# Kernel optimization log

Measured on AMD Instinct MI355X. Metric: run time of the kernel, lower is better.

Reference implementation:

```python
import jax, jax.numpy as jnp
import numpy as np

N = 50000
C_IN = 64
C_OUT = 64
K = 16
EPS = 1e-5


def _bn(x, g, b, m, v):
    # eval-mode BatchNorm1d over last dim
    return (x - m) * jax.lax.rsqrt(v + EPS) * g + b


def setup_inputs() -> dict:
    key = jax.random.key(0)
    ks = jax.random.split(key, 24)
    def lin(i, fan_in, fan_out):
        s = 1.0 / np.sqrt(fan_in)
        W = jax.random.uniform(ks[i], (fan_in, fan_out), jnp.float32, -s, s)
        b = jax.random.uniform(ks[i + 1], (fan_out,), jnp.float32, -s, s)
        return W, b
    Wq, bq = lin(0, C_IN, C_OUT)
    Wk, bk = lin(2, C_IN, C_OUT)
    Wv, bv = lin(4, C_IN, C_OUT)
    Wp, b_p = lin(6, 3, C_OUT)
    Wg1, bg1 = lin(8, C_OUT, C_OUT)
    Wg2, bg2 = lin(10, C_OUT, C_OUT)
    Wo, bo = lin(12, C_OUT, C_OUT)
    def bn_params(i):
        g = jax.random.uniform(ks[i], (C_OUT,), jnp.float32, 0.5, 1.5)
        b = jax.random.normal(ks[i + 1], (C_OUT,), jnp.float32) * 0.1
        m = jax.random.normal(ks[i + 2], (C_OUT,), jnp.float32) * 0.1
        v = jax.random.uniform(ks[i + 3], (C_OUT,), jnp.float32, 0.5, 1.5)
        return g, b, m, v
    bnp_g, bnp_b, bnp_m, bnp_v = bn_params(14)
    bng_g, bng_b, bng_m, bng_v = bn_params(18)
    points = jax.random.normal(ks[22], (N, 3), jnp.float32)
    features = jax.random.normal(ks[23], (N, C_IN), jnp.float32)
    grouped_indices = jax.random.randint(jax.random.fold_in(key, 7), (N, K), 0, N, jnp.int64 if jax.config.jax_enable_x64 else jnp.int32)
    return dict(points=points, features=features, grouped_indices=grouped_indices,
                Wq=Wq, bq=bq, Wk=Wk, bk=bk, Wv=Wv, bv=bv, Wp=Wp, b_p=b_p,
                bnp_g=bnp_g, bnp_b=bnp_b, bnp_m=bnp_m, bnp_v=bnp_v,
                Wg1=Wg1, bg1=bg1, bng_g=bng_g, bng_b=bng_b, bng_m=bng_m, bng_v=bng_v,
                Wg2=Wg2, bg2=bg2, Wo=Wo, bo=bo)


def reference(points, features, grouped_indices,
              Wq, bq, Wk, bk, Wv, bv, Wp, b_p,
              bnp_g, bnp_b, bnp_m, bnp_v,
              Wg1, bg1, bng_g, bng_b, bng_m, bng_v,
              Wg2, bg2, Wo, bo):
    q = features @ Wq + bq                      # (N, C)
    k = features @ Wk + bk
    v = features @ Wv + bv
    gpts = points[grouped_indices]              # (N, K, 3) gather
    gk = k[grouped_indices]                     # (N, K, C)
    gv = v[grouped_indices]                     # (N, K, C)
    rel = gpts - points[:, None, :]             # (N, K, 3)
    p = jax.nn.relu(_bn(rel @ Wp + b_p, bnp_g, bnp_b, bnp_m, bnp_v))  # (N, K, C)
    a = q[:, None, :] - gk + p                  # (N, K, C)
    h = jax.nn.relu(_bn(a @ Wg1 + bg1, bng_g, bng_b, bng_m, bng_v)) @ Wg2 + bg2
    attn = jax.nn.softmax(h, axis=1)            # softmax over neighbor axis
    out = jnp.sum((gv + p) * attn, axis=1) @ Wo + bo  # (N, C)
    return out
```

## Files before the change

kernel.cpp:

```cpp
#include <hip/hip_runtime.h>
#include <hip/hip_bf16.h>

#define EPSV 1e-5f
#define TW 4
#define TPW 8
#define SPD 76

typedef __attribute__((ext_vector_type(8))) short s8v;
typedef __attribute__((ext_vector_type(4))) float f4v;

struct InP {
  const float *points, *features; const int* gidx;
  const float *Wq,*bq,*Wk,*bk,*Wv,*bv,*Wp,*b_p;
  const float *bnp_g,*bnp_b,*bnp_m,*bnp_v;
  const float *Wg1,*bg1,*bng_g,*bng_b,*bng_m,*bng_v;
  const float *Wg2,*bg2,*Wo,*bo;
  float* out; int N;
};
struct WS {
  unsigned short *qW1;
  unsigned short *kvT;
  unsigned short *WAf, *Wkf, *Wvf, *W1f, *W2f, *Wof;
  unsigned short *Wpf;
  float *bq1F, *bpF, *bk1F;
};

__device__ __forceinline__ unsigned short f2bf(float x){
  __hip_bfloat16 h = __float2bfloat16(x);
  unsigned short u; __builtin_memcpy(&u, &h, 2); return u;
}
__device__ __forceinline__ float bf2f(unsigned short s){
  union{unsigned u; float f;} c; c.u = ((unsigned)s) << 16; return c.f;
}
__device__ __forceinline__ unsigned pk2(float x, float y){
  __hip_bfloat162 h = __float22bfloat162_rn(make_float2(x, y));
  unsigned u; __builtin_memcpy(&u, &h, 4); return u;
}
__device__ __forceinline__ s8v pack8(f4v x0, f4v x1){
  s8v r;
  ((unsigned*)&r)[0] = pk2(x0[0], x0[1]);
  ((unsigned*)&r)[1] = pk2(x0[2], x0[3]);
  ((unsigned*)&r)[2] = pk2(x1[0], x1[1]);
  ((unsigned*)&r)[3] = pk2(x1[2], x1[3]);
  return r;
}

__global__ void __launch_bounds__(256) prep_kernel(InP P, WS W){
  const int g = blockIdx.x*256 + threadIdx.x;
  const int e = g >> 3, j = g & 7;
  const int f = e >> 6, L = e & 63;
  const int ks = f & 1, nt = f >> 1;
  const int n = nt*16 + (L & 15);
  const int k = ks*32 + ((L >> 4) << 3) + j;
  const float sg = P.bng_g[n] * rsqrtf(P.bng_v[n] + EPSV);
  W.W1f[e*8+j] = f2bf(P.Wg1[k*64+n] * sg);
  W.W2f[e*8+j] = f2bf(P.Wg2[k*64+n]);
  W.Wof[e*8+j] = f2bf(P.Wo [k*64+n]);
  W.Wvf[e*8+j] = f2bf(P.Wv [k*64+n]);
  float acc = 0.f, acck = 0.f;
  #pragma unroll 8
  for (int d = 0; d < 64; d++){
    float w1 = P.Wg1[d*64+n];
    acc  += P.Wq[k*64+d] * w1;
    acck += P.Wk[k*64+d] * w1;
  }
  W.WAf[e*8+j] = f2bf(acc  * sg);
  W.Wkf[e*8+j] = f2bf(acck * sg);
  if (g < 2048){
    int ep = g >> 3;
    int ntp = ep >> 6, Lp = ep & 63;
    int np_ = ntp*16 + (Lp & 15);
    int kp = ((Lp >> 4) << 3) + j;
    float sp = P.bnp_g[np_] * rsqrtf(P.bnp_v[np_] + EPSV);
    W.Wpf[ep*8+j] = f2bf(kp < 3 ? P.Wp[kp*64+np_]*sp : 0.f);
  }
  if (g < 64){
    float sgt = P.bng_g[g] * rsqrtf(P.bng_v[g] + EPSV);
    float spt = P.bnp_g[g] * rsqrtf(P.bnp_v[g] + EPSV);
    float acc2 = 0.f, acck2 = 0.f;
    for (int d = 0; d < 64; d++){
      float w1 = P.Wg1[d*64+g];
      acc2  += P.bq[d] * w1;
      acck2 += P.bk[d] * w1;
    }
    W.bq1F[g] = acc2*sgt + P.bg1[g]*sgt + P.bng_b[g] - P.bng_m[g]*sgt;
    W.bk1F[g] = acck2*sgt;
    W.bpF[g]  = P.b_p[g]*spt + P.bnp_b[g] - P.bnp_m[g]*spt;
  }
}

__global__ void __launch_bounds__(256) qkv_kernel(InP P, WS W){
  const int tid = threadIdx.x;
  const int wid = tid >> 6, l = tid & 63;
  const int cl = l & 15, q = l >> 4;
  const int TILES = (P.N + 15) >> 4;
  const int task = blockIdx.x * TW + wid;
  if (task >= TILES) return;
  const int i0 = task * 16;
  int row = i0 + cl; if (row > P.N - 1) row = P.N - 1;
  const float* fr = P.features + (size_t)row*64 + q*8;
  f4v x0 = *(const f4v*)fr;
  f4v x1 = *(const f4v*)(fr + 4);
  s8v fa0 = pack8(x0, x1);
  x0 = *(const f4v*)(fr + 32);
  x1 = *(const f4v*)(fr + 36);
  s8v fa1 = pack8(x0, x1);

  auto doMat = [&](const unsigned short* Bf_, const float* biasPtr,
                   unsigned short* outPtr, int stride){
    const s8v* Bf = (const s8v*)Bf_;
    #pragma unroll
    for (int nt = 0; nt < 4; nt++){
      float bn = biasPtr[nt*16 + cl];
      f4v ci = { bn, bn, bn, bn };
      f4v c = __builtin_amdgcn_mfma_f32_16x16x32_bf16(fa0, Bf[(2*nt+0)*64 + l], ci, 0, 0, 0);
      c = __builtin_amdgcn_mfma_f32_16x16x32_bf16(fa1, Bf[(2*nt+1)*64 + l], c, 0, 0, 0);
      #pragma unroll
      for (int r = 0; r < 4; r++){
        int rg = i0 + q*4 + r;
        if (rg < P.N) outPtr[(size_t)rg*stride + nt*16 + cl] = f2bf(c[r]);
      }
    }
  };
  doMat(W.WAf, W.bq1F, W.qW1,      64);
  doMat(W.Wkf, W.bk1F, W.kvT,     128);
  doMat(W.Wvf, P.bv,   W.kvT + 64,128);
}

__global__ void __launch_bounds__(256, 2) main_kernel(InP P, WS W){
  __shared__ __align__(16) unsigned short Sp[TW][2][16*SPD];
  __shared__ __align__(16) unsigned short PreB[TW][TPW*SPD];
  __shared__ __align__(16) int sI[TW][TPW*16];
  const int tid = threadIdx.x;
  const int wid = tid >> 6, l = tid & 63;
  const int cl = l & 15, q = l >> 4;
  const int TILES = (P.N + TPW - 1) / TPW;
  const int task = blockIdx.x * TW + wid;
  if (task >= TILES) return;
  const int i0 = task * TPW;
  unsigned short* PreBw = PreB[wid];
  int* sIw = sI[wid];

  {
    long base = (long)i0*16 + l*2;
    long maxb = (long)P.N*16 - 2;
    if (base > maxb) base = maxb;
    int2 gi = *(const int2*)(P.gidx + base);
    *(int2*)&sIw[l*2] = gi;
  }

  s8v w1f[8], w2f[8], wpf[4];
  {
    const s8v* W1p = (const s8v*)W.W1f;
    const s8v* W2p = (const s8v*)W.W2f;
    const s8v* Wpp = (const s8v*)W.Wpf;
    #pragma unroll
    for (int f = 0; f < 8; f++){ w1f[f] = W1p[f*64 + l]; w2f[f] = W2p[f*64 + l]; }
    #pragma unroll
    for (int f = 0; f < 4; f++) wpf[f] = Wpp[f*64 + l];
  }
  float bp4[4], b24[4];
  #pragma unroll
  for (int nt = 0; nt < 4; nt++){ bp4[nt] = W.bpF[nt*16 + cl]; b24[nt] = P.bg2[nt*16 + cl]; }

  float ngx=0.f, ngy=0.f, ngz=0.f;
  {
    int nidx = sIw[cl];
    if (l < 16){ const float* gp = P.points + (size_t)nidx*3; ngx=gp[0]; ngy=gp[1]; ngz=gp[2]; }
  }
  float ncx = P.points[(size_t)i0*3+0];
  float ncy = P.points[(size_t)i0*3+1];
  float ncz = P.points[(size_t)i0*3+2];
  float nq0, nq1, nq2, nq3;
  {
    const unsigned short* qr = W.qW1 + (size_t)i0*64;
    nq0 = bf2f(qr[cl]); nq1 = bf2f(qr[16+cl]); nq2 = bf2f(qr[32+cl]); nq3 = bf2f(qr[48+cl]);
  }

  #pragma unroll 2
  for (int pt = 0; pt < TPW; pt++){
    unsigned short* Spw = Sp[wid][pt & 1];
    float gx=ngx, gy=ngy, gz=ngz, cx=ncx, cy=ncy, cz=ncz;
    float qcn4[4] = { nq0, nq1, nq2, nq3 };
    const bool valid = (i0 + pt < P.N);

    unsigned short kw[16], vv[16];
    {
      int4 vidx = *(const int4*)&sIw[pt*16 + q*4];
      #pragma unroll
      for (int r = 0; r < 4; r++){
        const unsigned short* vb = W.kvT + (size_t)vidx[r]*128 + cl;
        #pragma unroll
        for (int nt = 0; nt < 4; nt++){
          kw[nt*4+r] = vb[nt*16];
          vv[nt*4+r] = vb[64 + nt*16];
        }
      }
    }

    s8v ap;
    ((unsigned*)&ap)[0] = pk2(gx-cx, gy-cy);
    ((unsigned*)&ap)[1] = pk2(gz-cz, 0.f);
    ((unsigned*)&ap)[2] = 0u; ((unsigned*)&ap)[3] = 0u;
    f4v pc[4];
    #pragma unroll
    for (int nt = 0; nt < 4; nt++){
      f4v ci = { bp4[nt], bp4[nt], bp4[nt], bp4[nt] };
      pc[nt] = __builtin_amdgcn_mfma_f32_16x16x32_bf16(ap, wpf[nt], ci, 0, 0, 0);
    }
    #pragma unroll
    for (int nt = 0; nt < 4; nt++){
      #pragma unroll
      for (int r = 0; r < 4; r++){
        pc[nt][r] = fmaxf(pc[nt][r], 0.f);
        Spw[(q*4+r)*SPD + nt*16 + cl] = f2bf(pc[nt][r]);
      }
    }

    {
      int np = (pt + 1) & (TPW-1);
      int nidx = sIw[np*16 + cl];
      if (l < 16){ const float* gp = P.points + (size_t)nidx*3; ngx=gp[0]; ngy=gp[1]; ngz=gp[2]; }
      int ii = i0 + np; if (ii > P.N - 1) ii = P.N - 1;
      ncx = P.points[(size_t)ii*3+0];
      ncy = P.points[(size_t)ii*3+1];
      ncz = P.points[(size_t)ii*3+2];
      const unsigned short* qr = W.qW1 + (size_t)ii*64;
      nq0 = bf2f(qr[cl]); nq1 = bf2f(qr[16+cl]); nq2 = bf2f(qr[32+cl]); nq3 = bf2f(qr[48+cl]);
    }

    s8v af0 = *(const s8v*)&Spw[cl*SPD + q*8];
    s8v af1 = *(const s8v*)&Spw[cl*SPD + 32 + q*8];

    f4v tc[4];
    #pragma unroll
    for (int nt = 0; nt < 4; nt++){
      f4v ci = { qcn4[nt] - bf2f(kw[nt*4+0]),
                 qcn4[nt] - bf2f(kw[nt*4+1]),
                 qcn4[nt] - bf2f(kw[nt*4+2]),
                 qcn4[nt] - bf2f(kw[nt*4+3]) };
      tc[nt] = __builtin_amdgcn_mfma_f32_16x16x32_bf16(af0, w1f[2*nt+0], ci, 0, 0, 0);
      tc[nt] = __builtin_amdgcn_mfma_f32_16x16x32_bf16(af1, w1f[2*nt+1], tc[nt], 0, 0, 0);
      #pragma unroll
      for (int r = 0; r < 4; r++) tc[nt][r] = fmaxf(tc[nt][r], 0.f);
    }

    #pragma unroll
    for (int nt = 0; nt < 4; nt++)
      #pragma unroll
      for (int r = 0; r < 4; r++)
        Spw[(q*4+r)*SPD + nt*16 + cl] = f2bf(tc[nt][r]);
    s8v tf0 = *(const s8v*)&Spw[cl*SPD + q*8];
    s8v tf1 = *(const s8v*)&Spw[cl*SPD + 32 + q*8];

    f4v hc[4];
    #pragma unroll
    for (int nt = 0; nt < 4; nt++){
      f4v ci = { b24[nt], b24[nt], b24[nt], b24[nt] };
      hc[nt] = __builtin_amdgcn_mfma_f32_16x16x32_bf16(tf0, w2f[2*nt+0], ci, 0, 0, 0);
      hc[nt] = __builtin_amdgcn_mfma_f32_16x16x32_bf16(tf1, w2f[2*nt+1], hc[nt], 0, 0, 0);
    }

    float pre4[4];
    #pragma unroll
    for (int nt = 0; nt < 4; nt++){
      float s = 0.f, acc = 0.f;
      #pragma unroll
      for (int r = 0; r < 4; r++){
        float e2 = __expf(hc[nt][r]);
        s += e2;
        acc = fmaf(e2, bf2f(vv[nt*4+r]) + pc[nt][r], acc);
      }
      s += __shfl_xor(s, 16, 64);
      s += __shfl_xor(s, 32, 64);
      acc += __shfl_xor(acc, 16, 64);
      acc += __shfl_xor(acc, 32, 64);
      pre4[nt] = acc * __builtin_amdgcn_rcpf(s);
    }
    if (valid){
      float sa = (l & 16) ? pre4[1] : pre4[0];
      float sb = (l & 16) ? pre4[3] : pre4[2];
      PreBw[pt*SPD + l] = f2bf((l & 32) ? sb : sa);
    }
  }

  s8v wof[8];
  {
    const s8v* Wop = (const s8v*)W.Wof;
    #pragma unroll
    for (int f = 0; f < 8; f++) wof[f] = Wop[f*64 + l];
  }
  s8v ef0 = *(const s8v*)&PreBw[(cl & (TPW-1))*SPD + q*8];
  s8v ef1 = *(const s8v*)&PreBw[(cl & (TPW-1))*SPD + 32 + q*8];
  #pragma unroll
  for (int nt = 0; nt < 4; nt++){
    float bn = P.bo[nt*16 + cl];
    f4v ci = { bn, bn, bn, bn };
    f4v oc = __builtin_amdgcn_mfma_f32_16x16x32_bf16(ef0, wof[2*nt+0], ci, 0, 0, 0);
    oc = __builtin_amdgcn_mfma_f32_16x16x32_bf16(ef1, wof[2*nt+1], oc, 0, 0, 0);
    #pragma unroll
    for (int r = 0; r < 4; r++){
      int ro = q*4 + r;
      int rg = i0 + ro;
      if (ro < TPW && rg < P.N) P.out[(size_t)rg*64 + nt*16 + cl] = oc[r];
    }
  }
}

extern "C" void kernel_launch(void* const* d_in, const int* in_sizes, int n_in,
                              void* d_out, int out_size, void* d_ws, size_t ws_size,
                              hipStream_t stream){
  InP P;
  P.points   = (const float*)d_in[0];
  P.features = (const float*)d_in[1];
  P.gidx     = (const int*)d_in[2];
  P.Wq  = (const float*)d_in[3];  P.bq  = (const float*)d_in[4];
  P.Wk  = (const float*)d_in[5];  P.bk  = (const float*)d_in[6];
  P.Wv  = (const float*)d_in[7];  P.bv  = (const float*)d_in[8];
  P.Wp  = (const float*)d_in[9];  P.b_p = (const float*)d_in[10];
  P.bnp_g = (const float*)d_in[11]; P.bnp_b = (const float*)d_in[12];
  P.bnp_m = (const float*)d_in[13]; P.bnp_v = (const float*)d_in[14];
  P.Wg1 = (const float*)d_in[15]; P.bg1 = (const float*)d_in[16];
  P.bng_g = (const float*)d_in[17]; P.bng_b = (const float*)d_in[18];
  P.bng_m = (const float*)d_in[19]; P.bng_v = (const float*)d_in[20];
  P.Wg2 = (const float*)d_in[21]; P.bg2 = (const float*)d_in[22];
  P.Wo  = (const float*)d_in[23]; P.bo  = (const float*)d_in[24];
  P.out = (float*)d_out;
  const int N = in_sizes[0] / 3;
  P.N = N;

  WS W;
  char* w = (char*)d_ws;
  W.qW1 = (unsigned short*)w; w += (size_t)N*64*2;
  W.kvT = (unsigned short*)w; w += (size_t)N*128*2;
  W.WAf = (unsigned short*)w; w += 8*64*8*2;
  W.Wkf = (unsigned short*)w; w += 8*64*8*2;
  W.Wvf = (unsigned short*)w; w += 8*64*8*2;
  W.W1f = (unsigned short*)w; w += 8*64*8*2;
  W.W2f = (unsigned short*)w; w += 8*64*8*2;
  W.Wof = (unsigned short*)w; w += 8*64*8*2;
  W.Wpf = (unsigned short*)w; w += 4*64*8*2;
  W.bq1F = (float*)w; w += 256;
  W.bpF  = (float*)w; w += 256;
  W.bk1F = (float*)w; w += 256;

  const int TILES16 = (N + 15) / 16;
  const int grid16 = (TILES16 + TW - 1) / TW;
  const int TILESM = (N + TPW - 1) / TPW;
  const int gridM = (TILESM + TW - 1) / TW;
  hipLaunchKernelGGL(prep_kernel, dim3(16),     dim3(256), 0, stream, P, W);
  hipLaunchKernelGGL(qkv_kernel,  dim3(grid16), dim3(256), 0, stream, P, W);
  hipLaunchKernelGGL(main_kernel, dim3(gridM),  dim3(256), 0, stream, P, W);
}
```

Before: 209.1 us.

## Stage K/V neighbor gathers through LDS with vectorized prefetch of next point

Replaces the scalar 2-byte gathers of K and V rows with 16-byte vector loads per lane, staged into a per-wave LDS buffer (padded stride). The loads for the next point are issued one iteration ahead and held in registers, so gather latency overlaps with the current point's MFMA work. This cuts the number of global load instructions and improves coalescing. In exchange it uses more LDS and adds LDS reads per element, and the LDS write/read ordering depends on wave lockstep without an explicit barrier.

New measurement: 213.1 us. Within noise of the previous version (+1.9%).

```diff
diff --git a/kernel.cpp b/kernel.cpp
--- a/kernel.cpp
+++ b/kernel.cpp
@@ -5,8 +5,10 @@
 #define TW 4
 #define TPW 8
 #define SPD 76
+#define KVD 136
 
 typedef __attribute__((ext_vector_type(8))) short s8v;
+typedef __attribute__((ext_vector_type(8))) unsigned short u8v;
 typedef __attribute__((ext_vector_type(4))) float f4v;
 
 struct InP {
@@ -129,6 +131,7 @@
 
 __global__ void __launch_bounds__(256, 2) main_kernel(InP P, WS W){
   __shared__ __align__(16) unsigned short Sp[TW][2][16*SPD];
+  __shared__ __align__(16) unsigned short KV[TW][16*KVD];
   __shared__ __align__(16) unsigned short PreB[TW][TPW*SPD];
   __shared__ __align__(16) int sI[TW][TPW*16];
   const int tid = threadIdx.x;
@@ -139,6 +142,7 @@
   if (task >= TILES) return;
   const int i0 = task * TPW;
   unsigned short* PreBw = PreB[wid];
+  unsigned short* KVw = KV[wid];
   int* sIw = sI[wid];
 
   {
@@ -175,6 +179,13 @@
   {
     const unsigned short* qr = W.qW1 + (size_t)i0*64;
     nq0 = bf2f(qr[cl]); nq1 = bf2f(qr[16+cl]); nq2 = bf2f(qr[32+cl]); nq3 = bf2f(qr[48+cl]);
+  }
+
+  u8v gst[4];
+  #pragma unroll
+  for (int b = 0; b < 4; b++){
+    int rowIdx = sIw[b*4 + q];
+    gst[b] = *(const u8v*)(W.kvT + (size_t)rowIdx*128 + cl*8);
   }
 
   #pragma unroll 2
@@ -184,17 +195,15 @@
     float qcn4[4] = { nq0, nq1, nq2, nq3 };
     const bool valid = (i0 + pt < P.N);
 
-    unsigned short kw[16], vv[16];
-    {
-      int4 vidx = *(const int4*)&sIw[pt*16 + q*4];
-      #pragma unroll
-      for (int r = 0; r < 4; r++){
-        const unsigned short* vb = W.kvT + (size_t)vidx[r]*128 + cl;
-        #pragma unroll
-        for (int nt = 0; nt < 4; nt++){
-          kw[nt*4+r] = vb[nt*16];
-          vv[nt*4+r] = vb[64 + nt*16];
-        }
+    #pragma unroll
+    for (int b = 0; b < 4; b++)
+      *(u8v*)&KVw[(b*4 + q)*KVD + cl*8] = gst[b];
+
+    if (pt + 1 < TPW){
+      #pragma unroll
+      for (int b = 0; b < 4; b++){
+        int rowIdx = sIw[(pt+1)*16 + b*4 + q];
+        gst[b] = *(const u8v*)(W.kvT + (size_t)rowIdx*128 + cl*8);
       }
     }
 
@@ -235,10 +244,10 @@
     f4v tc[4];
     #pragma unroll
     for (int nt = 0; nt < 4; nt++){
-      f4v ci = { qcn4[nt] - bf2f(kw[nt*4+0]),
-                 qcn4[nt] - bf2f(kw[nt*4+1]),
-                 qcn4[nt] - bf2f(kw[nt*4+2]),
-                 qcn4[nt] - bf2f(kw[nt*4+3]) };
+      f4v ci = { qcn4[nt] - bf2f(KVw[(q*4+0)*KVD + nt*16 + cl]),
+                 qcn4[nt] - bf2f(KVw[(q*4+1)*KVD + nt*16 + cl]),
+                 qcn4[nt] - bf2f(KVw[(q*4+2)*KVD + nt*16 + cl]),
+                 qcn4[nt] - bf2f(KVw[(q*4+3)*KVD + nt*16 + cl]) };
       tc[nt] = __builtin_amdgcn_mfma_f32_16x16x32_bf16(af0, w1f[2*nt+0], ci, 0, 0, 0);
       tc[nt] = __builtin_amdgcn_mfma_f32_16x16x32_bf16(af1, w1f[2*nt+1], tc[nt], 0, 0, 0);
       #pragma unroll
@@ -269,7 +278,7 @@
       for (int r = 0; r < 4; r++){
         float e2 = __expf(hc[nt][r]);
         s += e2;
-        acc = fmaf(e2, bf2f(vv[nt*4+r]) + pc[nt][r], acc);
+        acc = fmaf(e2, bf2f(KVw[(q*4+r)*KVD + 64 + nt*16 + cl]) + pc[nt][r], acc);
       }
       s += __shfl_xor(s, 16, 64);
       s += __shfl_xor(s, 32, 64);
```
